# Kernel optimization log

Hardware: AMD Instinct MI355X
Metric: run time of the kernel (lower is better)

Reference implementation:

```python
import jax, jax.numpy as jnp
import numpy as np

B, A, NBH, F, G, H = 8, 512, 64, 128, 50, 8
DH = F // H
CUTOFF = 5.0


def setup_inputs() -> dict:
    key = jax.random.key(0)
    ks = jax.random.split(key, 13)
    x = jax.random.normal(ks[0], (B, A, F), jnp.float32)
    e = jax.random.normal(ks[1], (B, A, F), jnp.float32)
    t = jax.random.normal(ks[2], (B, F), jnp.float32)
    # distances in [0, 1.2*cutoff] so some pairs fall outside the cutoff
    r_ij = jax.random.uniform(ks[3], (B, A, NBH), jnp.float32) * (1.2 * CUTOFF)
    f_ij = jax.random.normal(ks[4], (B, A, NBH, G), jnp.float32)
    neighbors = jax.random.randint(ks[5], (B, A, NBH), 0, A, jnp.int32)
    neighbor_mask = jax.random.randint(ks[6], (B, A, NBH), 0, 2, jnp.int32).astype(bool)
    sF = 1.0 / np.sqrt(F).astype(np.float32)
    W_filt = jax.random.normal(ks[7], (G, F), jnp.float32) * (1.0 / np.sqrt(G).astype(np.float32))
    b_filt = jnp.zeros((F,), jnp.float32)
    Wq = jax.random.normal(ks[8], (F, F), jnp.float32) * sF
    Wk = jax.random.normal(ks[9], (F, F), jnp.float32) * sF
    Wv = jax.random.normal(ks[10], (F, F), jnp.float32) * sF
    Wo = jax.random.normal(ks[11], (F, F), jnp.float32) * sF
    bo = jnp.zeros((F,), jnp.float32)
    return dict(e=e, x=x, t=t, r_ij=r_ij, f_ij=f_ij,
                W_filt=W_filt, b_filt=b_filt, Wq=Wq, Wk=Wk, Wv=Wv, Wo=Wo, bo=bo,
                neighbors=neighbors, neighbor_mask=neighbor_mask)


def reference(e, x, t, r_ij, f_ij, W_filt, b_filt, Wq, Wk, Wv, Wo, bo,
              neighbors, neighbor_mask):
    # ---- filter network + cosine cutoff: W (B, A, NBH, F) ----
    W = f_ij @ W_filt + b_filt
    C = 0.5 * (jnp.cos(jnp.pi * r_ij / CUTOFF) + 1.0)
    C = C * (r_ij < CUTOFF).astype(x.dtype)           # (B, A, NBH)
    W = W * C[..., None]

    # ---- neighbor gather: nbh (B, A, NBH, F) ----
    bidx = jnp.arange(B)[:, None, None]
    nbh = x[bidx, neighbors]                           # irregular gather
    nbh = nbh * W                                      # filter-modulated messages

    # ---- EgoAttention: central atom queries its neighbors ----
    q = (x @ Wq).reshape(B, A, H, DH)                  # bahd
    k = (nbh @ Wk).reshape(B, A, NBH, H, DH)           # banhd
    v = (nbh @ Wv).reshape(B, A, NBH, H, DH)
    scale = np.float32(1.0 / np.sqrt(DH))
    scores = jnp.einsum('bahd,banhd->bahn', q, k) * scale
    scores = jnp.where(neighbor_mask[:, :, None, :], scores, jnp.float32(-1e9))
    attn = jax.nn.softmax(scores, axis=-1)             # over neighbors
    msg = jnp.einsum('bahn,banhd->bahd', attn, v).reshape(B, A, F)
    v_out = msg @ Wo + bo

    # ---- residual (apply_transition_function=False branch) ----
    return x + v_out
```

## Files before the change

kernel.cpp:

```cpp
#include <hip/hip_runtime.h>
#include <math.h>

#define BB 8
#define AA 512
#define NBH 64
#define FF 128
#define GG 50
#define CUTOFF 5.0f

typedef __attribute__((ext_vector_type(8)))  short bf16x8;
typedef __attribute__((ext_vector_type(4)))  float f32x4;
typedef __attribute__((ext_vector_type(16))) float f32x16;

#define MST 136
#define FST 72

#define WKV_ELEMS (4*8*64*8)
#define WQO_ELEMS (8*4*64*8)
#define WF_ELEMS  (4*4*64*8)

__device__ __forceinline__ short f2bf(float f) {
    union { float f; unsigned u; } v; v.f = f;
    unsigned r = v.u + 0x7fffu + ((v.u >> 16) & 1u);
    return (short)(r >> 16);
}

__device__ __forceinline__ int swz(int n) { return ((n >> 3) & 3) << 3; }

__device__ __forceinline__ float row16_sum(float x) {
    int t;
    t = __builtin_amdgcn_update_dpp(0, __float_as_int(x), 0x128, 0xf, 0xf, true); x += __int_as_float(t);
    t = __builtin_amdgcn_update_dpp(0, __float_as_int(x), 0x124, 0xf, 0xf, true); x += __int_as_float(t);
    t = __builtin_amdgcn_update_dpp(0, __float_as_int(x), 0x122, 0xf, 0xf, true); x += __int_as_float(t);
    t = __builtin_amdgcn_update_dpp(0, __float_as_int(x), 0x121, 0xf, 0xf, true); x += __int_as_float(t);
    return x;
}

__global__ void prep_kernel(const float* __restrict__ Wk,
                            const float* __restrict__ Wv,
                            const float* __restrict__ Wq,
                            const float* __restrict__ Wo,
                            const float* __restrict__ Wf,
                            short* __restrict__ ws)
{
    int gid = blockIdx.x * blockDim.x + threadIdx.x;
    if (gid < 2 * WKV_ELEMS) {
        const float* src = (gid < WKV_ELEMS) ? Wk : Wv;
        int idx = gid & (WKV_ELEMS - 1);
        int j = idx & 7, l = (idx >> 3) & 63, rest = idx >> 9;
        int s = rest & 7, w = rest >> 3;
        int k = 16 * s + ((l >> 5) << 3) + j;
        int n = 32 * w + (l & 31);
        ws[gid] = f2bf(src[k * FF + n]);
    } else if (gid < 2 * WKV_ELEMS + 2 * WQO_ELEMS) {
        int idx2 = gid - 2 * WKV_ELEMS;
        const float* src = (idx2 < WQO_ELEMS) ? Wq : Wo;
        int idx = idx2 & (WQO_ELEMS - 1);
        int j = idx & 7, l = (idx >> 3) & 63, rest = idx >> 9;
        int s = rest & 3, c = rest >> 2;
        int k = 32 * s + (l >> 4) * 8 + j;
        int n = 16 * c + (l & 15);
        ws[gid] = f2bf(src[k * FF + n]);
    } else {
        int idx = gid - 2 * WKV_ELEMS - 2 * WQO_ELEMS;
        int j = idx & 7, l = (idx >> 3) & 63, rest = idx >> 9;
        int s = rest & 3, w = rest >> 2;
        int k = 16 * s + ((l >> 5) << 3) + j;
        int n = 32 * w + (l & 31);
        ws[gid] = (k < GG) ? f2bf(Wf[k * FF + n]) : (short)0;
    }
}

__global__ __launch_bounds__(256, 4)
void tdt_main(const float* __restrict__ x,
              const float* __restrict__ r_ij,
              const float* __restrict__ f_ij,
              const float* __restrict__ b_filt,
              const float* __restrict__ bo,
              const int*   __restrict__ neighbors,
              const int*   __restrict__ nmask,
              const short* __restrict__ WkB,
              const short* __restrict__ WvB,
              const short* __restrict__ WqB,
              const short* __restrict__ WoB,
              const short* __restrict__ WfB,
              float* __restrict__ out)
{
    const int ba   = blockIdx.x;
    const int b    = ba >> 9;
    const int tid  = threadIdx.x;
    const int lane = tid & 63;
    const int w    = tid >> 6;
    const int l15  = lane & 15;
    const int quad = lane >> 4;
    const int l31  = lane & 31;
    const int w5_4 = (lane >> 5) * 4;

    __shared__ short M_s[NBH * MST];
    __shared__ short f_s[NBH * FST];
    __shared__ short x_bf[FF];
    __shared__ short msg_bf[FF];
    __shared__ float x_s[FF];
    __shared__ float C_s[NBH];
    __shared__ int   nbr_s[NBH];

    const float* xb  = x + (size_t)b * AA * FF;
    const size_t bao = (size_t)ba;

    unsigned long long mask64 = __ballot(nmask[bao * NBH + lane] != 0);

    if (tid < FF) {
        float xv = x[bao * FF + tid];
        x_s[tid]  = xv;
        x_bf[tid] = f2bf(xv);
    }
    if (tid < NBH) {
        float r = r_ij[bao * NBH + tid];
        float c = 0.5f * (__cosf((float)M_PI * r * (1.0f / CUTOFF)) + 1.0f);
        C_s[tid]   = (r < CUTOFF) ? c : 0.0f;
        nbr_s[tid] = neighbors[bao * NBH + tid];
    }
    {
        const float* frow = f_ij + bao * (size_t)(NBH * GG);
        int n = tid / 50;
        int g = tid - n * 50;
        for (int it = 0; it < 13; ++it) {
            int idx = tid + it * 256;
            if (idx < NBH * GG)
                f_s[n * FST + (g ^ swz(n))] = f2bf(frow[idx]);
            g += 6; n += 5;
            if (g >= 50) { g -= 50; n += 1; }
        }
        for (int idx = tid; idx < NBH * (64 - GG); idx += 256) {
            int nn = idx / 14;
            int gg = GG + (idx - nn * 14);
            f_s[nn * FST + (gg ^ swz(nn))] = 0;
        }
    }
    __syncthreads();

    float qv[2];
    {
        bf16x8 xa[4];
#pragma unroll
        for (int s = 0; s < 4; ++s)
            xa[s] = *(const bf16x8*)&x_bf[s * 32 + quad * 8];
#pragma unroll
        for (int ct = 0; ct < 2; ++ct) {
            int cg = 2 * w + ct;
            f32x4 z = {0.f, 0.f, 0.f, 0.f};
#pragma unroll
            for (int s = 0; s < 4; ++s) {
                bf16x8 bq = *(const bf16x8*)&WqB[((cg * 4 + s) * 64 + lane) * 8];
                z = __builtin_amdgcn_mfma_f32_16x16x32_bf16(xa[s], bq, z, 0, 0, 0);
            }
            qv[ct] = z[0];
        }
    }

    {
        f32x16 wacc[2];
#pragma unroll
        for (int mt = 0; mt < 2; ++mt)
#pragma unroll
            for (int r = 0; r < 16; ++r) wacc[mt][r] = 0.0f;
#pragma unroll
        for (int s = 0; s < 4; ++s) {
            bf16x8 bf = *(const bf16x8*)&WfB[((w * 4 + s) * 64 + lane) * 8];
            int kb = 16 * s + ((lane >> 5) << 3);
#pragma unroll
            for (int mt = 0; mt < 2; ++mt) {
                int m = 32 * mt + l31;
                bf16x8 fa = *(const bf16x8*)&f_s[m * FST + (kb ^ swz(m))];
                wacc[mt] = __builtin_amdgcn_mfma_f32_32x32x16_bf16(fa, bf, wacc[mt], 0, 0, 0);
            }
        }
        int   c    = 32 * w + l31;
        float bflt = b_filt[c];
#pragma unroll
        for (int mt = 0; mt < 2; ++mt) {
#pragma unroll
            for (int r = 0; r < 16; ++r) {
                int n = 32 * mt + (r & 3) + 8 * (r >> 2) + w5_4;
                float cn = C_s[n];
                float xv = xb[(size_t)nbr_s[n] * FF + c];
                M_s[n * MST + (c ^ swz(n))] = f2bf((wacc[mt][r] + bflt) * cn * xv);
            }
        }
    }
    __syncthreads();

    f32x16 kacc[2], vacc[2];
#pragma unroll
    for (int mt = 0; mt < 2; ++mt)
#pragma unroll
        for (int r = 0; r < 16; ++r) { kacc[mt][r] = 0.0f; vacc[mt][r] = 0.0f; }
#pragma unroll
    for (int s = 0; s < 8; ++s) {
        bf16x8 bk = *(const bf16x8*)&WkB[((w * 8 + s) * 64 + lane) * 8];
        bf16x8 bv = *(const bf16x8*)&WvB[((w * 8 + s) * 64 + lane) * 8];
        int kb = 16 * s + ((lane >> 5) << 3);
#pragma unroll
        for (int mt = 0; mt < 2; ++mt) {
            int m = 32 * mt + l31;
            bf16x8 ma = *(const bf16x8*)&M_s[m * MST + (kb ^ swz(m))];
            kacc[mt] = __builtin_amdgcn_mfma_f32_32x32x16_bf16(ma, bk, kacc[mt], 0, 0, 0);
            vacc[mt] = __builtin_amdgcn_mfma_f32_32x32x16_bf16(ma, bv, vacc[mt], 0, 0, 0);
        }
    }

    {
        float qvm = qv[(lane >> 4) & 1];
        float sc[2][16];
#pragma unroll
        for (int mt = 0; mt < 2; ++mt) {
#pragma unroll
            for (int r = 0; r < 16; ++r) {
                float s = kacc[mt][r] * qvm;
                s = row16_sum(s);
                int n = 32 * mt + (r & 3) + 8 * (r >> 2) + w5_4;
                s *= 0.25f;
                sc[mt][r] = ((mask64 >> n) & 1ull) ? s : -1e9f;
            }
        }
        float mx = -1e30f;
#pragma unroll
        for (int mt = 0; mt < 2; ++mt)
#pragma unroll
            for (int r = 0; r < 16; ++r) mx = fmaxf(mx, sc[mt][r]);
        mx = fmaxf(mx, __shfl_xor(mx, 32, 64));
        float sum = 0.0f;
#pragma unroll
        for (int mt = 0; mt < 2; ++mt)
#pragma unroll
            for (int r = 0; r < 16; ++r) {
                float e = __expf(sc[mt][r] - mx);
                sc[mt][r] = e;
                sum += e;
            }
        sum += __shfl_xor(sum, 32, 64);
        float inv = 1.0f / sum;
        float acc = 0.0f;
#pragma unroll
        for (int mt = 0; mt < 2; ++mt)
#pragma unroll
            for (int r = 0; r < 16; ++r)
                acc = fmaf(sc[mt][r], vacc[mt][r], acc);
        acc += __shfl_xor(acc, 32, 64);
        if (lane < 32) msg_bf[32 * w + l31] = f2bf(acc * inv);
    }
    __syncthreads();

    {
        bf16x8 mga[4];
#pragma unroll
        for (int s = 0; s < 4; ++s)
            mga[s] = *(const bf16x8*)&msg_bf[s * 32 + quad * 8];
#pragma unroll
        for (int ct = 0; ct < 2; ++ct) {
            int cg = 2 * w + ct;
            f32x4 z = {0.f, 0.f, 0.f, 0.f};
#pragma unroll
            for (int s = 0; s < 4; ++s) {
                bf16x8 bw = *(const bf16x8*)&WoB[((cg * 4 + s) * 64 + lane) * 8];
                z = __builtin_amdgcn_mfma_f32_16x16x32_bf16(mga[s], bw, z, 0, 0, 0);
            }
            if (quad == 0) {
                int col = cg * 16 + l15;
                out[bao * FF + col] = z[0] + x_s[col] + bo[col];
            }
        }
    }
}

extern "C" void kernel_launch(void* const* d_in, const int* in_sizes, int n_in,
                              void* d_out, int out_size, void* d_ws, size_t ws_size,
                              hipStream_t stream) {
    const float* x      = (const float*)d_in[1];
    const float* r_ij   = (const float*)d_in[3];
    const float* f_ij   = (const float*)d_in[4];
    const float* W_filt = (const float*)d_in[5];
    const float* b_filt = (const float*)d_in[6];
    const float* Wq     = (const float*)d_in[7];
    const float* Wk     = (const float*)d_in[8];
    const float* Wv     = (const float*)d_in[9];
    const float* Wo     = (const float*)d_in[10];
    const float* bo     = (const float*)d_in[11];
    const int*   nbr    = (const int*)d_in[12];
    const int*   msk    = (const int*)d_in[13];
    float* out = (float*)d_out;

    short* ws  = (short*)d_ws;
    short* WkB = ws;
    short* WvB = ws + WKV_ELEMS;
    short* WqB = ws + 2 * WKV_ELEMS;
    short* WoB = ws + 2 * WKV_ELEMS + WQO_ELEMS;
    short* WfB = ws + 2 * WKV_ELEMS + 2 * WQO_ELEMS;

    int prep_total = 2 * WKV_ELEMS + 2 * WQO_ELEMS + WF_ELEMS;
    hipLaunchKernelGGL(prep_kernel, dim3(prep_total / 256), dim3(256), 0, stream,
                       Wk, Wv, Wq, Wo, W_filt, ws);
    hipLaunchKernelGGL(tdt_main, dim3(BB * AA), dim3(256), 0, stream,
                       x, r_ij, f_ij, b_filt, bo, nbr, msk,
                       WkB, WvB, WqB, WoB, WfB, out);
}
```

Before: 176.9 us.

## Load f_ij and x directly into MFMA fragments, split K/V phases, raise occupancy

Removes the shared-memory staging of f_ij, x, cutoff values and neighbor indices. MFMA operands are now loaded straight from global memory with float2 loads, and per-neighbor scalars are broadcast with wave shuffles. This drops the first __syncthreads and cuts LDS usage. The K and V projections are split so V is computed per m-tile after the softmax, which lowers live accumulator registers, and launch bounds are raised to 6 blocks per CU. The trade-off is that f_ij global loads are now uncoalesced (row stride of 50 floats, 8-byte loads that may be misaligned), and the 16 shuffles per wave add ALU work.

```diff
diff --git a/kernel.cpp b/kernel.cpp
--- a/kernel.cpp
+++ b/kernel.cpp
@@ -13,7 +13,6 @@
 typedef __attribute__((ext_vector_type(16))) float f32x16;
 
 #define MST 136
-#define FST 72
 
 #define WKV_ELEMS (4*8*64*8)
 #define WQO_ELEMS (8*4*64*8)
@@ -26,6 +25,15 @@
 }
 
 __device__ __forceinline__ int swz(int n) { return ((n >> 3) & 3) << 3; }
+
+__device__ __forceinline__ bf16x8 ld_f8_bf(const float* p) {
+    const float2* p2 = (const float2*)p;
+    float2 a = p2[0], b = p2[1], c = p2[2], d = p2[3];
+    bf16x8 r;
+    r[0] = f2bf(a.x); r[1] = f2bf(a.y); r[2] = f2bf(b.x); r[3] = f2bf(b.y);
+    r[4] = f2bf(c.x); r[5] = f2bf(c.y); r[6] = f2bf(d.x); r[7] = f2bf(d.y);
+    return r;
+}
 
 __device__ __forceinline__ float row16_sum(float x) {
     int t;
@@ -71,7 +79,7 @@
     }
 }
 
-__global__ __launch_bounds__(256, 4)
+__global__ __launch_bounds__(256, 6)
 void tdt_main(const float* __restrict__ x,
               const float* __restrict__ r_ij,
               const float* __restrict__ f_ij,
@@ -94,65 +102,36 @@
     const int l15  = lane & 15;
     const int quad = lane >> 4;
     const int l31  = lane & 31;
-    const int w5_4 = (lane >> 5) * 4;
+    const int khalf = (lane >> 5) << 3;
+    const int w5_4  = (lane >> 5) * 4;
 
     __shared__ short M_s[NBH * MST];
-    __shared__ short f_s[NBH * FST];
-    __shared__ short x_bf[FF];
     __shared__ short msg_bf[FF];
-    __shared__ float x_s[FF];
-    __shared__ float C_s[NBH];
-    __shared__ int   nbr_s[NBH];
-
-    const float* xb  = x + (size_t)b * AA * FF;
-    const size_t bao = (size_t)ba;
-
+
+    const float* xrow = x + (size_t)ba * FF;
+    const float* xb   = x + (size_t)b * AA * FF;
+    const size_t bao  = (size_t)ba;
+
+    int   nbr_reg = neighbors[bao * NBH + lane];
+    float C_reg;
+    {
+        float r = r_ij[bao * NBH + lane];
+        float c = 0.5f * (__cosf((float)M_PI * r * (1.0f / CUTOFF)) + 1.0f);
+        C_reg = (r < CUTOFF) ? c : 0.0f;
+    }
     unsigned long long mask64 = __ballot(nmask[bao * NBH + lane] != 0);
 
-    if (tid < FF) {
-        float xv = x[bao * FF + tid];
-        x_s[tid]  = xv;
-        x_bf[tid] = f2bf(xv);
-    }
-    if (tid < NBH) {
-        float r = r_ij[bao * NBH + tid];
-        float c = 0.5f * (__cosf((float)M_PI * r * (1.0f / CUTOFF)) + 1.0f);
-        C_s[tid]   = (r < CUTOFF) ? c : 0.0f;
-        nbr_s[tid] = neighbors[bao * NBH + tid];
-    }
-    {
-        const float* frow = f_ij + bao * (size_t)(NBH * GG);
-        int n = tid / 50;
-        int g = tid - n * 50;
-        for (int it = 0; it < 13; ++it) {
-            int idx = tid + it * 256;
-            if (idx < NBH * GG)
-                f_s[n * FST + (g ^ swz(n))] = f2bf(frow[idx]);
-            g += 6; n += 5;
-            if (g >= 50) { g -= 50; n += 1; }
-        }
-        for (int idx = tid; idx < NBH * (64 - GG); idx += 256) {
-            int nn = idx / 14;
-            int gg = GG + (idx - nn * 14);
-            f_s[nn * FST + (gg ^ swz(nn))] = 0;
-        }
-    }
-    __syncthreads();
-
     float qv[2];
     {
-        bf16x8 xa[4];
-#pragma unroll
-        for (int s = 0; s < 4; ++s)
-            xa[s] = *(const bf16x8*)&x_bf[s * 32 + quad * 8];
 #pragma unroll
         for (int ct = 0; ct < 2; ++ct) {
             int cg = 2 * w + ct;
             f32x4 z = {0.f, 0.f, 0.f, 0.f};
 #pragma unroll
             for (int s = 0; s < 4; ++s) {
+                bf16x8 xa = ld_f8_bf(xrow + 32 * s + quad * 8);
                 bf16x8 bq = *(const bf16x8*)&WqB[((cg * 4 + s) * 64 + lane) * 8];
-                z = __builtin_amdgcn_mfma_f32_16x16x32_bf16(xa[s], bq, z, 0, 0, 0);
+                z = __builtin_amdgcn_mfma_f32_16x16x32_bf16(xa, bq, z, 0, 0, 0);
             }
             qv[ct] = z[0];
         }
@@ -164,62 +143,68 @@
         for (int mt = 0; mt < 2; ++mt)
 #pragma unroll
             for (int r = 0; r < 16; ++r) wacc[mt][r] = 0.0f;
+
+        const float* fm0 = f_ij + bao * (size_t)(NBH * GG) + (size_t)l31 * GG;
 #pragma unroll
         for (int s = 0; s < 4; ++s) {
-            bf16x8 bf = *(const bf16x8*)&WfB[((w * 4 + s) * 64 + lane) * 8];
-            int kb = 16 * s + ((lane >> 5) << 3);
+            bf16x8 bfw = *(const bf16x8*)&WfB[((w * 4 + s) * 64 + lane) * 8];
+#pragma unroll
+            for (int mt = 0; mt < 2; ++mt) {
+                const float* fm = fm0 + mt * 32 * GG;
+                bf16x8 fa;
+                if (s < 3) {
+                    fa = ld_f8_bf(fm + 16 * s + khalf);
+                } else {
+#pragma unroll
+                    for (int jj = 0; jj < 8; ++jj) fa[jj] = 0;
+                    if (lane < 32) { fa[0] = f2bf(fm[48]); fa[1] = f2bf(fm[49]); }
+                }
+                wacc[mt] = __builtin_amdgcn_mfma_f32_32x32x16_bf16(fa, bfw, wacc[mt], 0, 0, 0);
+            }
+        }
+
+        int   c    = 32 * w + l31;
+        float bflt = b_filt[c];
+#pragma unroll
+        for (int mt = 0; mt < 2; ++mt) {
+#pragma unroll
+            for (int r = 0; r < 16; ++r) {
+                int   n   = 32 * mt + (r & 3) + 8 * (r >> 2) + w5_4;
+                int   nbn = __shfl(nbr_reg, n, 64);
+                float cn  = __shfl(C_reg, n, 64);
+                float xv  = xb[(size_t)nbn * FF + c];
+                M_s[n * MST + (c ^ swz(n))] = f2bf((wacc[mt][r] + bflt) * cn * xv);
+            }
+        }
+    }
+    __syncthreads();
+
+    float sc[2][16];
+    float inv;
+    {
+        f32x16 kacc[2];
+#pragma unroll
+        for (int mt = 0; mt < 2; ++mt)
+#pragma unroll
+            for (int r = 0; r < 16; ++r) kacc[mt][r] = 0.0f;
+#pragma unroll
+        for (int s = 0; s < 8; ++s) {
+            bf16x8 bk = *(const bf16x8*)&WkB[((w * 8 + s) * 64 + lane) * 8];
+            int kb = 16 * s + khalf;
 #pragma unroll
             for (int mt = 0; mt < 2; ++mt) {
                 int m = 32 * mt + l31;
-                bf16x8 fa = *(const bf16x8*)&f_s[m * FST + (kb ^ swz(m))];
-                wacc[mt] = __builtin_amdgcn_mfma_f32_32x32x16_bf16(fa, bf, wacc[mt], 0, 0, 0);
-            }
-        }
-        int   c    = 32 * w + l31;
-        float bflt = b_filt[c];
+                bf16x8 ma = *(const bf16x8*)&M_s[m * MST + (kb ^ swz(m))];
+                kacc[mt] = __builtin_amdgcn_mfma_f32_32x32x16_bf16(ma, bk, kacc[mt], 0, 0, 0);
+            }
+        }
+        float qvm = qv[(lane >> 4) & 1];
 #pragma unroll
         for (int mt = 0; mt < 2; ++mt) {
 #pragma unroll
             for (int r = 0; r < 16; ++r) {
+                float s = row16_sum(kacc[mt][r] * qvm) * 0.25f;
                 int n = 32 * mt + (r & 3) + 8 * (r >> 2) + w5_4;
-                float cn = C_s[n];
-                float xv = xb[(size_t)nbr_s[n] * FF + c];
-                M_s[n * MST + (c ^ swz(n))] = f2bf((wacc[mt][r] + bflt) * cn * xv);
-            }
-        }
-    }
-    __syncthreads();
-
-    f32x16 kacc[2], vacc[2];
-#pragma unroll
-    for (int mt = 0; mt < 2; ++mt)
-#pragma unroll
-        for (int r = 0; r < 16; ++r) { kacc[mt][r] = 0.0f; vacc[mt][r] = 0.0f; }
-#pragma unroll
-    for (int s = 0; s < 8; ++s) {
-        bf16x8 bk = *(const bf16x8*)&WkB[((w * 8 + s) * 64 + lane) * 8];
-        bf16x8 bv = *(const bf16x8*)&WvB[((w * 8 + s) * 64 + lane) * 8];
-        int kb = 16 * s + ((lane >> 5) << 3);
-#pragma unroll
-        for (int mt = 0; mt < 2; ++mt) {
-            int m = 32 * mt + l31;
-            bf16x8 ma = *(const bf16x8*)&M_s[m * MST + (kb ^ swz(m))];
-            kacc[mt] = __builtin_amdgcn_mfma_f32_32x32x16_bf16(ma, bk, kacc[mt], 0, 0, 0);
-            vacc[mt] = __builtin_amdgcn_mfma_f32_32x32x16_bf16(ma, bv, vacc[mt], 0, 0, 0);
-        }
-    }
-
-    {
-        float qvm = qv[(lane >> 4) & 1];
-        float sc[2][16];
-#pragma unroll
-        for (int mt = 0; mt < 2; ++mt) {
-#pragma unroll
-            for (int r = 0; r < 16; ++r) {
-                float s = kacc[mt][r] * qvm;
-                s = row16_sum(s);
-                int n = 32 * mt + (r & 3) + 8 * (r >> 2) + w5_4;
-                s *= 0.25f;
                 sc[mt][r] = ((mask64 >> n) & 1ull) ? s : -1e9f;
             }
         }
@@ -239,13 +224,28 @@
                 sum += e;
             }
         sum += __shfl_xor(sum, 32, 64);
-        float inv = 1.0f / sum;
+        inv = 1.0f / sum;
+    }
+
+    {
         float acc = 0.0f;
 #pragma unroll
-        for (int mt = 0; mt < 2; ++mt)
+        for (int mt = 0; mt < 2; ++mt) {
+            f32x16 vacc;
+#pragma unroll
+            for (int r = 0; r < 16; ++r) vacc[r] = 0.0f;
+            int m = 32 * mt + l31;
+#pragma unroll
+            for (int s = 0; s < 8; ++s) {
+                bf16x8 bv = *(const bf16x8*)&WvB[((w * 8 + s) * 64 + lane) * 8];
+                int kb = 16 * s + khalf;
+                bf16x8 ma = *(const bf16x8*)&M_s[m * MST + (kb ^ swz(m))];
+                vacc = __builtin_amdgcn_mfma_f32_32x32x16_bf16(ma, bv, vacc, 0, 0, 0);
+            }
 #pragma unroll
             for (int r = 0; r < 16; ++r)
-                acc = fmaf(sc[mt][r], vacc[mt][r], acc);
+                acc = fmaf(sc[mt][r], vacc[r], acc);
+        }
         acc += __shfl_xor(acc, 32, 64);
         if (lane < 32) msg_bf[32 * w + l31] = f2bf(acc * inv);
     }
@@ -267,7 +267,7 @@
             }
             if (quad == 0) {
                 int col = cg * 16 + l15;
-                out[bao * FF + col] = z[0] + x_s[col] + bo[col];
+                out[bao * FF + col] = z[0] + xrow[col] + bo[col];
             }
         }
     }
```

Result: slower. 323.3 us (+82.7%).
